# Kernel optimization log

Hardware: AMD Instinct MI355X
Metric: run time of the kernel (lower is better)

The kernel has to match this reference:

```python
import jax, jax.numpy as jnp
import numpy as np

MAX_DISP = 20  # matches init_kwargs max_displacement


def setup_inputs() -> dict:
    key = jax.random.key(0)
    k1, k2 = jax.random.split(key)
    feat1 = jax.random.normal(k1, (4, 128, 64, 64), dtype=jnp.float32)
    feat2 = jax.random.normal(k2, (4, 128, 64, 64), dtype=jnp.float32)
    return {"feat1": feat1, "feat2": feat2}


def reference(feat1, feat2):
    pad = MAX_DISP
    D = 2 * pad + 1  # displacement window side (41)
    b, c, h, w = feat1.shape
    feat2_pad = jnp.pad(feat2, ((0, 0), (0, 0), (pad, pad), (pad, pad)))

    def step(carry, ij):
        i = ij // D
        j = ij % D
        sl = jax.lax.dynamic_slice(feat2_pad, (0, 0, i, j), (b, c, h, w))
        # dot over channel dim -> [b, h, w]
        return carry, jnp.sum(feat1 * sl, axis=1)

    # scan over all D*D displacements keeps peak memory at one [b,c,h,w] slice
    _, corr = jax.lax.scan(step, None, jnp.arange(D * D))  # [D*D, b, h, w]
    return jnp.transpose(corr, (1, 0, 2, 3))  # [b, D*D, h, w]
```

## Files before the change

### kernel.cpp

```cpp
#include <hip/hip_runtime.h>
#include <stdint.h>


#define NB 4
#define NC 128
#define NH 64
#define NW 64
#define PAD 20
#define ND 41
#define HW (NH * NW)
#define ROW_U4 1024

typedef __attribute__((ext_vector_type(8))) __bf16 bf16x8;
typedef __attribute__((ext_vector_type(16))) float f32x16;

__device__ __forceinline__ unsigned int pk2(float a, float b) {
  unsigned short lo = __builtin_bit_cast(unsigned short, (__bf16)a);
  unsigned short hi = __builtin_bit_cast(unsigned short, (__bf16)b);
  return (unsigned int)lo | ((unsigned int)hi << 16);
}

__global__ __launch_bounds__(256) void conv_kernel(
    const float* __restrict__ f1, const float* __restrict__ f2,
    uint4* __restrict__ ws) {
  const int blk = blockIdx.x;
  const int isF2 = blk >> 8;
  const int by = blk & 255;
  const int b = by >> 6, y = by & 63;
  const float* src = (isF2 ? f2 : f1) + (size_t)b * NC * HW + (size_t)y * NW;
  uint4* dst = ws + (size_t)isF2 * (NB * NH * ROW_U4) + (size_t)by * ROW_U4;
  const int x = threadIdx.x & 63;
  const int cq = threadIdx.x >> 6;
#pragma unroll
  for (int it = 0; it < 4; ++it) {
    const int cg = it * 4 + cq;
    float v[8];
#pragma unroll
    for (int i = 0; i < 8; ++i) v[i] = src[(size_t)(cg * 8 + i) * HW + x];
    uint4 u;
    u.x = pk2(v[0], v[1]);
    u.y = pk2(v[2], v[3]);
    u.z = pk2(v[4], v[5]);
    u.w = pk2(v[6], v[7]);
    dst[cg * 64 + x] = u;
  }
}

__global__ __launch_bounds__(256, 4) void corr_main(
    const uint4* __restrict__ ws, float* __restrict__ out) {
  __shared__ float cbuf[2][64 * 64];

  const int bid = blockIdx.x;
  const int lid = (bid & 7) * 128 + (bid >> 3);
  const int dq = lid & 3;
  const int y = (lid >> 2) & 63;
  const int b = lid >> 8;

  const int t = threadIdx.x;
  const int lane = t & 63;
  const int wv = t >> 6;
  const int I = wv & 1;
  const int J = wv >> 1;
  const int kh = lane >> 5;

  const int xa = I * 32 + (lane & 31);
  const int xb = J * 32 + (lane & 31);
  const int col = (lane & 31) + 32 * J;
  const int rbase = kh * 4 + I * 32;
  const int xg = t & 63;
  const int g = t >> 6;

  const uint4* f1t = ws;
  const uint4* f2t = ws + NB * NH * ROW_U4;

  const int dBeg = (ND * dq) / 4;
  const int dEnd = (ND * (dq + 1)) / 4;
  int a0 = 20 - y;
  if (a0 < dBeg) a0 = dBeg;
  if (a0 > dEnd) a0 = dEnd;
  int a1 = 84 - y;
  if (a1 < a0) a1 = a0;
  if (a1 > dEnd) a1 = dEnd;

  const size_t outBase = (size_t)b * (ND * ND) * HW + (size_t)y * NW;

  for (int di = dBeg; di < a0; ++di) {
    const size_t dB = outBase + (size_t)di * ND * HW;
    for (int k = g; k < ND; k += 4)
      __builtin_nontemporal_store(0.f, &out[dB + (size_t)k * HW + xg]);
  }
  for (int di = a1; di < dEnd; ++di) {
    const size_t dB = outBase + (size_t)di * ND * HW;
    for (int k = g; k < ND; k += 4)
      __builtin_nontemporal_store(0.f, &out[dB + (size_t)k * HW + xg]);
  }
  const int n = a1 - a0;
  if (n <= 0) return;

  const uint4* f1row = f1t + (size_t)(b * 64 + y) * ROW_U4 + kh * 64 + xb;
  bf16x8 bfrag[8];
#pragma unroll
  for (int ks = 0; ks < 8; ++ks)
    bfrag[ks] = __builtin_bit_cast(bf16x8, f1row[ks * 128]);

  const uint4* f2row = f2t + (size_t)(b * 64) * ROW_U4 + kh * 64 + xa;

  int p = 0;
#pragma unroll 1
  for (int j = 0; j < n; ++j) {
    const int yp = y + (a0 + j) - PAD;
    const uint4* ap = f2row + (size_t)yp * ROW_U4;
    uint4 a[8];
#pragma unroll
    for (int ks = 0; ks < 8; ++ks) a[ks] = ap[ks * 128];

    if (j > 0) {
      const size_t dB = outBase + (size_t)(a0 + j - 1) * ND * HW;
      const float* cb = cbuf[p ^ 1];
      for (int k = g; k < ND; k += 4) {
        const int xs = xg + k - PAD;
        const float vv = (xs >= 0 && xs < NW) ? cb[xs * 64 + xg] : 0.f;
        __builtin_nontemporal_store(vv, &out[dB + (size_t)k * HW + xg]);
      }
    }

    f32x16 acc;
#pragma unroll
    for (int r = 0; r < 16; ++r) acc[r] = 0.f;
#pragma unroll
    for (int ks = 0; ks < 8; ++ks)
      acc = __builtin_amdgcn_mfma_f32_32x32x16_bf16(
          __builtin_bit_cast(bf16x8, a[ks]), bfrag[ks], acc, 0, 0, 0);
#pragma unroll
    for (int r = 0; r < 16; ++r) {
      const int row = rbase + (r & 3) + 8 * (r >> 2);
      cbuf[p][row * 64 + col] = acc[r];
    }
    __syncthreads();
    p ^= 1;
  }

  {
    const size_t dB = outBase + (size_t)(a0 + n - 1) * ND * HW;
    const float* cb = cbuf[p ^ 1];
    for (int k = g; k < ND; k += 4) {
      const int xs = xg + k - PAD;
      const float vv = (xs >= 0 && xs < NW) ? cb[xs * 64 + xg] : 0.f;
      __builtin_nontemporal_store(vv, &out[dB + (size_t)k * HW + xg]);
    }
  }
}

__device__ __forceinline__ float f4elem(const float4 v, int j) {
  return j == 0 ? v.x : j == 1 ? v.y : j == 2 ? v.z : v.w;
}

__device__ __forceinline__ void convwrite(const float4 (&v)[8],
                                          uint4* __restrict__ lds, int xq,
                                          int cg) {
#pragma unroll
  for (int j = 0; j < 4; ++j) {
    const int x = xq * 4 + j;
    uint4 u;
    u.x = pk2(f4elem(v[0], j), f4elem(v[1], j));
    u.y = pk2(f4elem(v[2], j), f4elem(v[3], j));
    u.z = pk2(f4elem(v[4], j), f4elem(v[5], j));
    u.w = pk2(f4elem(v[6], j), f4elem(v[7], j));
    lds[x * 16 + (cg ^ (x & 7))] = u;
  }
}

__global__ __launch_bounds__(256, 2) void corr_fallback(
    const float* __restrict__ feat1, const float* __restrict__ feat2,
    float* __restrict__ out) {
  __shared__ uint4 f2s[2][64 * 16];
  __shared__ float cbuf[2][64 * 64];

  const int bid = blockIdx.x;
  const int lid = (bid & 7) * 64 + (bid >> 3);
  const int half = lid & 1;
  const int y = (lid >> 1) & 63;
  const int b = lid >> 7;

  const int t = threadIdx.x;
  const int lane = t & 63;
  const int wv = t >> 6;
  const int I = wv & 1;
  const int J = wv >> 1;
  const int xa = I * 32 + (lane & 31);
  const int xb = J * 32 + (lane & 31);
  const int kh = lane >> 5;
  const int aBase = xa * 16, aSw = xa & 7;
  const int bBase = xb * 16, bSw = xb & 7;
  const int col = (lane & 31) + J * 32;
  const int rbase = kh * 4 + I * 32;
  const int xg = t & 63;
  const int g = t >> 6;
  const int xq = t & 15;
  const int cg = t >> 4;
  const size_t rowoff = (size_t)cg * 8 * HW + xq * 4;
  const float* f1row = feat1 + (size_t)b * NC * HW + (size_t)y * NW + rowoff;
  const float* f2row0 = feat2 + (size_t)b * NC * HW + rowoff;
  const size_t outBase = ((size_t)b * (ND * ND) * NH + y) * NW;

  int dBeg, dEnd;
  if (half == 0) {
    dBeg = (y < PAD) ? (PAD - y) : 0;
    dEnd = PAD + 1;
  } else {
    dBeg = PAD + 1;
    const int e = (NH + PAD) - y;
    dEnd = e < ND ? e : ND;
  }
  const int zBeg = half ? dEnd : 0;
  const int zEnd = half ? ND : dBeg;
  for (int di = zBeg; di < zEnd; ++di) {
    const size_t dB = outBase + (size_t)di * ND * HW;
    for (int k = g; k < ND; k += 4)
      __builtin_nontemporal_store(0.f, &out[dB + (size_t)k * HW + xg]);
  }
  if (dBeg >= dEnd) return;

  float4 v[8];
#pragma unroll
  for (int i = 0; i < 8; ++i) v[i] = *(const float4*)(f1row + (size_t)i * HW);
  uint4* f1tmp = (uint4*)&cbuf[0][0];
  convwrite(v, f1tmp, xq, cg);
  {
    const int yp0 = y + dBeg - PAD;
#pragma unroll
    for (int i = 0; i < 8; ++i)
      v[i] = *(const float4*)(f2row0 + (size_t)yp0 * NW + (size_t)i * HW);
  }
  __syncthreads();
  bf16x8 bfrag[8];
#pragma unroll
  for (int ks = 0; ks < 8; ++ks) {
    const int q = ks * 2 + kh;
    bfrag[ks] = __builtin_bit_cast(bf16x8, f1tmp[bBase + (q ^ bSw)]);
  }
  __syncthreads();

  const int nIter = dEnd - dBeg;
  int p = 0;
#pragma unroll 1
  for (int j = 0; j < nIter; ++j) {
    convwrite(v, f2s[p], xq, cg);
    {
      const int nj = (j + 1 < nIter) ? j + 1 : j;
      const int ypn = y + dBeg + nj - PAD;
#pragma unroll
      for (int i = 0; i < 8; ++i)
        v[i] = *(const float4*)(f2row0 + (size_t)ypn * NW + (size_t)i * HW);
    }
    __syncthreads();

    f32x16 acc;
#pragma unroll
    for (int r = 0; r < 16; ++r) acc[r] = 0.f;
#pragma unroll
    for (int ks = 0; ks < 8; ++ks) {
      const int q = ks * 2 + kh;
      bf16x8 aa = __builtin_bit_cast(bf16x8, f2s[p][aBase + (q ^ aSw)]);
      acc = __builtin_amdgcn_mfma_f32_32x32x16_bf16(aa, bfrag[ks], acc, 0, 0, 0);
    }
#pragma unroll
    for (int r = 0; r < 16; ++r) {
      const int row = rbase + (r & 3) + 8 * (r >> 2);
      cbuf[p][row * 64 + col] = acc[r];
    }
    if (j > 0) {
      const size_t dBase = outBase + (size_t)(dBeg + j - 1) * ND * HW;
      const float* cb = cbuf[p ^ 1];
      for (int k = g; k < ND; k += 4) {
        const int xs = xg + k - PAD;
        const float vv = (xs >= 0 && xs < NW) ? cb[xs * 64 + xg] : 0.f;
        __builtin_nontemporal_store(vv, &out[dBase + (size_t)k * HW + xg]);
      }
    }
    p ^= 1;
  }
  __syncthreads();
  {
    const size_t dBase = outBase + (size_t)(dEnd - 1) * ND * HW;
    const float* cb = cbuf[p ^ 1];
    for (int k = g; k < ND; k += 4) {
      const int xs = xg + k - PAD;
      const float vv = (xs >= 0 && xs < NW) ? cb[xs * 64 + xg] : 0.f;
      __builtin_nontemporal_store(vv, &out[dBase + (size_t)k * HW + xg]);
    }
  }
}

extern "C" void kernel_launch(void* const* d_in, const int* in_sizes, int n_in,
                              void* d_out, int out_size, void* d_ws,
                              size_t ws_size, hipStream_t stream) {
  (void)in_sizes; (void)n_in; (void)out_size;
  const float* f1 = (const float*)d_in[0];
  const float* f2 = (const float*)d_in[1];
  float* out = (float*)d_out;
  const size_t need = (size_t)2 * NB * NH * ROW_U4 * sizeof(uint4);
  if (ws_size >= need && d_ws != nullptr) {
    uint4* ws = (uint4*)d_ws;
    conv_kernel<<<dim3(512), dim3(256), 0, stream>>>(f1, f2, ws);
    corr_main<<<dim3(NB * NH * 4), dim3(256), 0, stream>>>(ws, out);
  } else {
    corr_fallback<<<dim3(NB * NH * 2), dim3(256), 0, stream>>>(f1, f2, out);
  }
}
```

Measured before the change: 38.13 us.

## Vectorize conversion loads, use lighter LDS barrier, and plain stores in fallback

The conversion kernel now has each thread load float4 vectors across 8 channels and pack four bf16x8 outputs, replacing scalar loads. The main kernel's per-iteration __syncthreads is replaced by an explicit lgkmcnt wait plus s_barrier, which does not wait on outstanding global stores. The fallback kernel switches from nontemporal to ordinary stores and changes its A-fragment swizzle index from aSw to bSw. That last change can alter correctness if the two swizzles differ, and the barrier change depends on no global-memory ordering being needed across the barrier.

```diff
diff --git a/kernel.cpp b/kernel.cpp
--- a/kernel.cpp
+++ b/kernel.cpp
@@ -14,10 +14,20 @@
 typedef __attribute__((ext_vector_type(8))) __bf16 bf16x8;
 typedef __attribute__((ext_vector_type(16))) float f32x16;
 
+__device__ __forceinline__ void barrier_lds() {
+  asm volatile("s_waitcnt lgkmcnt(0)" ::: "memory");
+  __builtin_amdgcn_s_barrier();
+  asm volatile("" ::: "memory");
+}
+
 __device__ __forceinline__ unsigned int pk2(float a, float b) {
   unsigned short lo = __builtin_bit_cast(unsigned short, (__bf16)a);
   unsigned short hi = __builtin_bit_cast(unsigned short, (__bf16)b);
   return (unsigned int)lo | ((unsigned int)hi << 16);
+}
+
+__device__ __forceinline__ float f4elem(const float4 v, int j) {
+  return j == 0 ? v.x : j == 1 ? v.y : j == 2 ? v.z : v.w;
 }
 
 __global__ __launch_bounds__(256) void conv_kernel(
@@ -29,20 +39,20 @@
   const int b = by >> 6, y = by & 63;
   const float* src = (isF2 ? f2 : f1) + (size_t)b * NC * HW + (size_t)y * NW;
   uint4* dst = ws + (size_t)isF2 * (NB * NH * ROW_U4) + (size_t)by * ROW_U4;
-  const int x = threadIdx.x & 63;
-  const int cq = threadIdx.x >> 6;
-#pragma unroll
-  for (int it = 0; it < 4; ++it) {
-    const int cg = it * 4 + cq;
-    float v[8];
-#pragma unroll
-    for (int i = 0; i < 8; ++i) v[i] = src[(size_t)(cg * 8 + i) * HW + x];
+  const int xq = threadIdx.x & 15;
+  const int cg = threadIdx.x >> 4;
+  const float* p = src + (size_t)cg * 8 * HW + xq * 4;
+  float4 v[8];
+#pragma unroll
+  for (int i = 0; i < 8; ++i) v[i] = *(const float4*)(p + (size_t)i * HW);
+#pragma unroll
+  for (int j = 0; j < 4; ++j) {
     uint4 u;
-    u.x = pk2(v[0], v[1]);
-    u.y = pk2(v[2], v[3]);
-    u.z = pk2(v[4], v[5]);
-    u.w = pk2(v[6], v[7]);
-    dst[cg * 64 + x] = u;
+    u.x = pk2(f4elem(v[0], j), f4elem(v[1], j));
+    u.y = pk2(f4elem(v[2], j), f4elem(v[3], j));
+    u.z = pk2(f4elem(v[4], j), f4elem(v[5], j));
+    u.w = pk2(f4elem(v[6], j), f4elem(v[7], j));
+    dst[cg * 64 + xq * 4 + j] = u;
   }
 }
 
@@ -136,7 +146,7 @@
       const int row = rbase + (r & 3) + 8 * (r >> 2);
       cbuf[p][row * 64 + col] = acc[r];
     }
-    __syncthreads();
+    barrier_lds();
     p ^= 1;
   }
 
@@ -149,10 +159,6 @@
       __builtin_nontemporal_store(vv, &out[dB + (size_t)k * HW + xg]);
     }
   }
-}
-
-__device__ __forceinline__ float f4elem(const float4 v, int j) {
-  return j == 0 ? v.x : j == 1 ? v.y : j == 2 ? v.z : v.w;
 }
 
 __device__ __forceinline__ void convwrite(const float4 (&v)[8],
@@ -216,8 +222,7 @@
   const int zEnd = half ? ND : dBeg;
   for (int di = zBeg; di < zEnd; ++di) {
     const size_t dB = outBase + (size_t)di * ND * HW;
-    for (int k = g; k < ND; k += 4)
-      __builtin_nontemporal_store(0.f, &out[dB + (size_t)k * HW + xg]);
+    for (int k = g; k < ND; k += 4) out[dB + (size_t)k * HW + xg] = 0.f;
   }
   if (dBeg >= dEnd) return;
 
@@ -261,7 +266,7 @@
 #pragma unroll
     for (int ks = 0; ks < 8; ++ks) {
       const int q = ks * 2 + kh;
-      bf16x8 aa = __builtin_bit_cast(bf16x8, f2s[p][aBase + (q ^ aSw)]);
+      bf16x8 aa = __builtin_bit_cast(bf16x8, f2s[p][aBase + (q ^ bSw)]);
       acc = __builtin_amdgcn_mfma_f32_32x32x16_bf16(aa, bfrag[ks], acc, 0, 0, 0);
     }
 #pragma unroll
@@ -275,7 +280,7 @@
       for (int k = g; k < ND; k += 4) {
         const int xs = xg + k - PAD;
         const float vv = (xs >= 0 && xs < NW) ? cb[xs * 64 + xg] : 0.f;
-        __builtin_nontemporal_store(vv, &out[dBase + (size_t)k * HW + xg]);
+        out[dBase + (size_t)k * HW + xg] = vv;
       }
     }
     p ^= 1;
@@ -287,7 +292,7 @@
     for (int k = g; k < ND; k += 4) {
       const int xs = xg + k - PAD;
       const float vv = (xs >= 0 && xs < NW) ? cb[xs * 64 + xg] : 0.f;
-      __builtin_nontemporal_store(vv, &out[dBase + (size_t)k * HW + xg]);
+      out[dBase + (size_t)k * HW + xg] = vv;
     }
   }
 }
```

New measurement: 39.94 us. 1.05x slower.
